# Kernel tuning notes

Measured on AMD Instinct MI355X. Metric: run time of the kernel, lower is better.

## Reference

```python
import jax, jax.numpy as jnp
import numpy as np

B, N, D, E, H, K = 2, 2048, 1024, 8, 2048, 2


def setup_inputs() -> dict:
    key = jax.random.key(0)
    ks = jax.random.split(key, 5)
    s = 0.02  # init scale
    return {
        "x": jax.random.normal(ks[0], (B, N, D), dtype=jnp.float32),
        "w_gate": jax.random.normal(ks[1], (D, E), dtype=jnp.float32) * s,
        "b_gate": jnp.zeros((E,), dtype=jnp.float32),
        "w1": jax.random.normal(ks[2], (E, D, H), dtype=jnp.float32) * s,
        "b1": jnp.zeros((E, H), dtype=jnp.float32),
        "w2": jax.random.normal(ks[3], (E, H, D), dtype=jnp.float32) * s,
        "b2": jnp.zeros((E, D), dtype=jnp.float32),
    }


def reference(x, w_gate, b_gate, w1, b1, w2, b2):
    b, n, d = x.shape
    T = b * n
    xf = x.reshape(T, d)                                   # (T, D)
    # --- top-k routing ---
    logits = xf @ w_gate + b_gate                          # (T, E)
    topk_logits, topk_idx = jax.lax.top_k(logits, K)       # (T, K)
    topk_gates = jax.nn.softmax(topk_logits, axis=-1)      # softmax over selected experts
    entropy = -(topk_gates * jnp.log(jnp.clip(topk_gates, 1e-8, None))).sum(-1).mean()
    # scatter top-k gates into full (T, E) gate matrix (zeros for unselected)
    gates = jnp.zeros_like(logits).at[jnp.arange(T)[:, None], topk_idx].add(topk_gates)
    # --- expert MLPs (dense over experts; gates zero out unselected) ---
    h = jax.nn.relu(jnp.einsum('td,edh->eth', xf, w1) + b1[:, None, :])  # (E, T, H)
    y = jnp.einsum('eth,ehd->etd', h, w2) + b2[:, None, :]               # (E, T, D)
    out = jnp.einsum('etd,te->td', y, gates).reshape(b, n, d)
    return out, entropy
```

## Files before the change

kernel.cpp:

```cpp
#include <hip/hip_runtime.h>

#define T_TOK 4096
#define D_DIM 1024
#define E_EXP 8
#define H_DIM 2048
#define CAP   9216
#define TILES_M 72

typedef __attribute__((ext_vector_type(8))) short bf16x8;
typedef __attribute__((ext_vector_type(4))) float f32x4;

__device__ inline unsigned short f2bf(float f) {
    unsigned int u = __float_as_uint(f);
    unsigned int r = (u + 0x7fffu + ((u >> 16) & 1u)) >> 16;
    return (unsigned short)r;
}

#define GLD_LDS16(g, l)                                                        \
    __builtin_amdgcn_global_load_lds(                                          \
        (const __attribute__((address_space(1))) void*)(g),                    \
        (__attribute__((address_space(3))) void*)(l), 16, 0, 0)

__global__ __launch_bounds__(256) void tcvt_kernel(const float* __restrict__ src,
                                                   unsigned short* __restrict__ dst,
                                                   int R, int C) {
    __shared__ float tile[64][65];
    size_t eo = (size_t)blockIdx.z * R * C;
    src += eo; dst += eo;
    int tx = threadIdx.x & 15, ty = threadIdx.x >> 4;
    int c0 = blockIdx.x * 64, r0 = blockIdx.y * 64;
    #pragma unroll
    for (int i = 0; i < 4; i++) {
        int row = ty + i * 16;
        float4 v = *(const float4*)&src[(size_t)(r0 + row) * C + c0 + tx * 4];
        tile[row][tx * 4 + 0] = v.x;
        tile[row][tx * 4 + 1] = v.y;
        tile[row][tx * 4 + 2] = v.z;
        tile[row][tx * 4 + 3] = v.w;
    }
    __syncthreads();
    #pragma unroll
    for (int i = 0; i < 4; i++) {
        int cc = ty + i * 16;
        int rr = tx * 4;
        ushort4 o;
        o.x = f2bf(tile[rr + 0][cc]);
        o.y = f2bf(tile[rr + 1][cc]);
        o.z = f2bf(tile[rr + 2][cc]);
        o.w = f2bf(tile[rr + 3][cc]);
        *(ushort4*)&dst[(size_t)(c0 + cc) * R + r0 + rr] = o;
    }
}

__global__ __launch_bounds__(256) void gating_kernel(
    const float* __restrict__ xf, const float* __restrict__ wg,
    const float* __restrict__ bg, unsigned short* __restrict__ xb,
    int* __restrict__ tk_e, float* __restrict__ tk_g,
    float* __restrict__ ent_part)
{
    __shared__ float ents[4];
    int wave = threadIdx.x >> 6, lane = threadIdx.x & 63;
    int t = blockIdx.x * 4 + wave;
    const float* xr = xf + (size_t)t * D_DIM;
    unsigned short* xbr = xb + (size_t)t * D_DIM;
    float acc[8] = {0.f,0.f,0.f,0.f,0.f,0.f,0.f,0.f};
    for (int i = 0; i < 16; i++) {
        int d = lane + i * 64;
        float xv = xr[d];
        xbr[d] = f2bf(xv);
        const float4* wr = (const float4*)(wg + (size_t)d * 8);
        float4 w0 = wr[0], w1 = wr[1];
        acc[0] += xv * w0.x; acc[1] += xv * w0.y; acc[2] += xv * w0.z; acc[3] += xv * w0.w;
        acc[4] += xv * w1.x; acc[5] += xv * w1.y; acc[6] += xv * w1.z; acc[7] += xv * w1.w;
    }
    #pragma unroll
    for (int s = 1; s < 64; s <<= 1) {
        #pragma unroll
        for (int e = 0; e < 8; e++) acc[e] += __shfl_xor(acc[e], s, 64);
    }
    if (lane == 0) {
        float l[8];
        #pragma unroll
        for (int e = 0; e < 8; e++) l[e] = acc[e] + bg[e];
        int i0 = 0;
        #pragma unroll
        for (int e = 1; e < 8; e++) if (l[e] > l[i0]) i0 = e;
        int i1 = (i0 == 0) ? 1 : 0;
        #pragma unroll
        for (int e = 0; e < 8; e++) if (e != i0 && l[e] > l[i1]) i1 = e;
        float z  = expf(l[i1] - l[i0]);
        float p0 = 1.0f / (1.0f + z);
        float p1 = z / (1.0f + z);
        float ent = -(p0 * logf(fmaxf(p0, 1e-8f)) + p1 * logf(fmaxf(p1, 1e-8f)));
        ents[wave] = ent;
        tk_e[t * 2 + 0] = i0; tk_g[t * 2 + 0] = p0;
        tk_e[t * 2 + 1] = i1; tk_g[t * 2 + 1] = p1;
    }
    __syncthreads();
    if (threadIdx.x == 0)
        ent_part[blockIdx.x] = ents[0] + ents[1] + ents[2] + ents[3];
}

__global__ __launch_bounds__(1024) void route_kernel(
    const int* __restrict__ tk_e, const float* __restrict__ tk_g,
    int* __restrict__ off, int* __restrict__ slot_token,
    float* __restrict__ slot_gate, int* __restrict__ slot_of,
    const float* __restrict__ ent_part, float* __restrict__ ent_out)
{
    __shared__ int wt[16][8];
    __shared__ int wx[16][8];
    __shared__ int base[9];
    __shared__ int tot[8];
    __shared__ float es[16];

    int tid = threadIdx.x, wid = tid >> 6, lane = tid & 63;
    int i0 = tid * 8;
    int ev[8];
    *(int4*)&ev[0] = *(const int4*)&tk_e[i0];
    *(int4*)&ev[4] = *(const int4*)&tk_e[i0 + 4];

    float s = ent_part[tid];
    #pragma unroll
    for (int d = 1; d < 64; d <<= 1) s += __shfl_xor(s, d, 64);
    if (lane == 0) es[wid] = s;

    unsigned own[4] = {0u, 0u, 0u, 0u};
    #pragma unroll
    for (int j = 0; j < 8; j++) {
        int e = ev[j];
        int reg = ((e < 4) ? 0 : 2) + (e & 1);
        own[reg] += 1u << (((e >> 1) & 1) * 16);
    }
    unsigned inc[4] = {own[0], own[1], own[2], own[3]};
    #pragma unroll
    for (int d = 1; d < 64; d <<= 1) {
        #pragma unroll
        for (int k = 0; k < 4; k++) {
            unsigned t = __shfl_up(inc[k], d, 64);
            if (lane >= d) inc[k] += t;
        }
    }
    if (lane == 63) {
        #pragma unroll
        for (int e = 0; e < 8; e++) {
            int reg = ((e < 4) ? 0 : 2) + (e & 1);
            wt[wid][e] = (inc[reg] >> (((e >> 1) & 1) * 16)) & 0xFFFF;
        }
    }
    __syncthreads();
    if (tid == 0) {
        int o = 0;
        for (int e = 0; e < 8; e++) {
            int run = 0;
            for (int w = 0; w < 16; w++) { wx[w][e] = run; run += wt[w][e]; }
            tot[e] = run;
            base[e] = o;
            off[e] = o;
            o += (run + 127) & ~127;
        }
        base[8] = o;
        off[8] = o;
        float se = 0.f;
        for (int w = 0; w < 16; w++) se += es[w];
        *ent_out = se * (1.0f / T_TOK);
    }
    __syncthreads();

    #pragma unroll
    for (int e = 0; e < 8; e++) {
        int p0 = base[e] + tot[e], p1 = base[e + 1];
        for (int i = p0 + tid; i < p1; i += 1024) slot_token[i] = -1;
    }

    unsigned run[4] = {0u, 0u, 0u, 0u};
    #pragma unroll
    for (int j = 0; j < 8; j++) {
        int e = ev[j];
        int reg = ((e < 4) ? 0 : 2) + (e & 1);
        int sh = ((e >> 1) & 1) * 16;
        int lx = (int)(((inc[reg] - own[reg]) >> sh) & 0xFFFF);
        int lr = (int)((run[reg] >> sh) & 0xFFFF);
        int slot = base[e] + wx[wid][e] + lx + lr;
        run[reg] += 1u << sh;
        int i = i0 + j;
        slot_token[slot] = i >> 1;
        slot_gate[slot] = tk_g[i];
        slot_of[i] = slot;
    }
}

template<int KD, int ND, bool GATHER, bool RELU>
__global__ __launch_bounds__(256) void gemm2p_kernel(
    const unsigned short* __restrict__ Ag, const unsigned short* __restrict__ Bw,
    const float* __restrict__ bias, const int* __restrict__ off,
    const int* __restrict__ slot_token, unsigned short* __restrict__ Out)
{
    __shared__ __align__(16) unsigned short As[2][128 * 32];
    __shared__ __align__(16) unsigned short Bs[2][128 * 32];

    int nwgx = gridDim.x;
    int nwg = nwgx * gridDim.y;
    int orig = blockIdx.y * nwgx + blockIdx.x;
    int q = nwg >> 3, r = nwg & 7;
    int xcd = orig & 7, idx = orig >> 3;
    int nid = (xcd < r ? xcd * (q + 1) : r * (q + 1) + (xcd - r) * q) + idx;
    int bx = nid % nwgx, by = nid / nwgx;

    int s0 = bx * 128;
    if (s0 >= off[E_EXP]) return;
    int e = 0;
    while (s0 >= off[e + 1]) e++;
    int n0 = by * 128;

    int tid = threadIdx.x;
    int wave = tid >> 6, lane = tid & 63;
    int lrow = lane & 15, quad = lane >> 4;
    int srow = lane >> 2;
    int scol = ((lane & 3) ^ ((srow >> 1) & 3)) * 8;

    int r0 = 16 * wave + srow, r1 = r0 + 64;
    const unsigned short* a0;
    const unsigned short* a1;
    if constexpr (GATHER) {
        int t0 = slot_token[s0 + r0]; if (t0 < 0) t0 = 0;
        int t1 = slot_token[s0 + r1]; if (t1 < 0) t1 = 0;
        a0 = Ag + (size_t)t0 * KD + scol;
        a1 = Ag + (size_t)t1 * KD + scol;
    } else {
        a0 = Ag + (size_t)(s0 + r0) * KD + scol;
        a1 = Ag + (size_t)(s0 + r1) * KD + scol;
    }
    const unsigned short* wb = Bw + (size_t)e * ND * KD;
    const unsigned short* bp0 = wb + (size_t)(n0 + r0) * KD + scol;
    const unsigned short* bp1 = wb + (size_t)(n0 + r1) * KD + scol;

    int stA0 = (16 * wave) * 32;
    int stA1 = (64 + 16 * wave) * 32;

    f32x4 acc[4][4];
    #pragma unroll
    for (int mi = 0; mi < 4; mi++)
        #pragma unroll
        for (int ni = 0; ni < 4; ni++) acc[mi][ni] = (f32x4){0.f, 0.f, 0.f, 0.f};

    int wr = (wave >> 1) * 64, wc = (wave & 1) * 64;
    int g = (quad ^ ((lrow >> 1) & 3)) * 8;

    GLD_LDS16(a0,  &As[0][stA0]);
    GLD_LDS16(a1,  &As[0][stA1]);
    GLD_LDS16(bp0, &Bs[0][stA0]);
    GLD_LDS16(bp1, &Bs[0][stA1]);
    __syncthreads();

    constexpr int NT = KD / 32;
    int cur = 0;
    for (int t = 0; t < NT - 1; ++t) {
        int nb = cur ^ 1;
        int k1 = (t + 1) * 32;
        GLD_LDS16(a0 + k1,  &As[nb][stA0]);
        GLD_LDS16(a1 + k1,  &As[nb][stA1]);
        GLD_LDS16(bp0 + k1, &Bs[nb][stA0]);
        GLD_LDS16(bp1 + k1, &Bs[nb][stA1]);
        bf16x8 af[4], bfr[4];
        #pragma unroll
        for (int i = 0; i < 4; i++) {
            af[i]  = *(const bf16x8*)&As[cur][(wr + i * 16 + lrow) * 32 + g];
            bfr[i] = *(const bf16x8*)&Bs[cur][(wc + i * 16 + lrow) * 32 + g];
        }
        #pragma unroll
        for (int mi = 0; mi < 4; mi++)
            #pragma unroll
            for (int ni = 0; ni < 4; ni++)
                acc[mi][ni] = __builtin_amdgcn_mfma_f32_16x16x32_bf16(
                    af[mi], bfr[ni], acc[mi][ni], 0, 0, 0);
        __syncthreads();
        cur = nb;
    }
    {
        bf16x8 af[4], bfr[4];
        #pragma unroll
        for (int i = 0; i < 4; i++) {
            af[i]  = *(const bf16x8*)&As[cur][(wr + i * 16 + lrow) * 32 + g];
            bfr[i] = *(const bf16x8*)&Bs[cur][(wc + i * 16 + lrow) * 32 + g];
        }
        #pragma unroll
        for (int mi = 0; mi < 4; mi++)
            #pragma unroll
            for (int ni = 0; ni < 4; ni++)
                acc[mi][ni] = __builtin_amdgcn_mfma_f32_16x16x32_bf16(
                    af[mi], bfr[ni], acc[mi][ni], 0, 0, 0);
    }

    float bv[4];
    #pragma unroll
    for (int ni = 0; ni < 4; ni++)
        bv[ni] = bias[(size_t)e * ND + n0 + wc + ni * 16 + lrow];
    unsigned short* w = &As[0][0] + wave * 1024;
    __syncthreads();
    #pragma unroll
    for (int mi = 0; mi < 4; mi++) {
        #pragma unroll
        for (int ni = 0; ni < 4; ni++)
            #pragma unroll
            for (int rr = 0; rr < 4; rr++) {
                float v = acc[mi][ni][rr] + bv[ni];
                if constexpr (RELU) v = fmaxf(v, 0.0f);
                w[(quad * 4 + rr) * 64 + ni * 16 + lrow] = f2bf(v);
            }
        int rd = lane >> 3, cc = (lane & 7) * 8;
        bf16x8 v0 = *(const bf16x8*)&w[rd * 64 + cc];
        bf16x8 v1 = *(const bf16x8*)&w[(8 + rd) * 64 + cc];
        size_t rowg = (size_t)(s0 + wr + mi * 16 + rd) * ND + n0 + wc + cc;
        *(bf16x8*)&Out[rowg] = v0;
        *(bf16x8*)&Out[rowg + 8 * (size_t)ND] = v1;
    }
}

__global__ __launch_bounds__(256) void combine_kernel(
    const unsigned short* __restrict__ Yb, const int* __restrict__ slot_of,
    const float* __restrict__ tk_g, float* __restrict__ out)
{
    int t = blockIdx.x * 2 + (threadIdx.x >> 7);
    int j = threadIdx.x & 127;
    int sA = slot_of[t * 2], sB = slot_of[t * 2 + 1];
    float gA = tk_g[t * 2], gB = tk_g[t * 2 + 1];
    uint4 va = *(const uint4*)(Yb + (size_t)sA * D_DIM + j * 8);
    uint4 vb = *(const uint4*)(Yb + (size_t)sB * D_DIM + j * 8);
    const unsigned int* pa = (const unsigned int*)&va;
    const unsigned int* pb = (const unsigned int*)&vb;
    float o[8];
    #pragma unroll
    for (int i = 0; i < 4; i++) {
        float a_lo = __uint_as_float(pa[i] << 16);
        float a_hi = __uint_as_float(pa[i] & 0xffff0000u);
        float b_lo = __uint_as_float(pb[i] << 16);
        float b_hi = __uint_as_float(pb[i] & 0xffff0000u);
        o[i * 2 + 0] = gA * a_lo + gB * b_lo;
        o[i * 2 + 1] = gA * a_hi + gB * b_hi;
    }
    float* op = out + (size_t)t * D_DIM + j * 8;
    ((float4*)op)[0] = make_float4(o[0], o[1], o[2], o[3]);
    ((float4*)op)[1] = make_float4(o[4], o[5], o[6], o[7]);
}

extern "C" void kernel_launch(void* const* d_in, const int* in_sizes, int n_in,
                              void* d_out, int out_size, void* d_ws, size_t ws_size,
                              hipStream_t stream)
{
    const float* xf = (const float*)d_in[0];
    const float* wg = (const float*)d_in[1];
    const float* bg = (const float*)d_in[2];
    const float* w1 = (const float*)d_in[3];
    const float* b1 = (const float*)d_in[4];
    const float* w2 = (const float*)d_in[5];
    const float* b2 = (const float*)d_in[6];
    float* out = (float*)d_out;

    char* p = (char*)d_ws;
    int* off    = (int*)p;
    int* tk_e   = off + 16;
    float* tk_g = (float*)(tk_e + T_TOK * 2);
    int* slot_token = (int*)(tk_g + T_TOK * 2);
    float* slot_gate = (float*)(slot_token + CAP);
    int* slot_of = (int*)(slot_gate + CAP);
    float* ent_part = (float*)(slot_of + T_TOK * 2);
    size_t ofs = ((size_t)((char*)(ent_part + T_TOK / 4) - p) + 255) & ~(size_t)255;
    unsigned short* xb  = (unsigned short*)(p + ofs); ofs += (size_t)T_TOK * D_DIM * 2;
    unsigned short* w1t = (unsigned short*)(p + ofs); ofs += (size_t)E_EXP * D_DIM * H_DIM * 2;
    unsigned short* w2t = (unsigned short*)(p + ofs); ofs += (size_t)E_EXP * H_DIM * D_DIM * 2;
    unsigned short* Hb  = (unsigned short*)(p + ofs); ofs += (size_t)CAP * H_DIM * 2;
    unsigned short* Yb  = w1t;

    gating_kernel<<<T_TOK / 4, 256, 0, stream>>>(xf, wg, bg, xb, tk_e, tk_g, ent_part);
    route_kernel<<<1, 1024, 0, stream>>>(tk_e, tk_g, off, slot_token, slot_gate, slot_of,
                                         ent_part, out + (size_t)T_TOK * D_DIM);
    tcvt_kernel<<<dim3(H_DIM / 64, D_DIM / 64, E_EXP), 256, 0, stream>>>(w1, w1t, D_DIM, H_DIM);
    tcvt_kernel<<<dim3(D_DIM / 64, H_DIM / 64, E_EXP), 256, 0, stream>>>(w2, w2t, H_DIM, D_DIM);
    gemm2p_kernel<D_DIM, H_DIM, true, true>
        <<<dim3(TILES_M, H_DIM / 128), 256, 0, stream>>>(xb, w1t, b1, off, slot_token, Hb);
    gemm2p_kernel<H_DIM, D_DIM, false, false>
        <<<dim3(TILES_M, D_DIM / 128), 256, 0, stream>>>(Hb, w2t, b2, off, slot_token, Yb);
    combine_kernel<<<T_TOK / 2, 256, 0, stream>>>(Yb, slot_of, tk_g, out);
}
```

Measured before the change: 371.1 us.

## Deepen grouped GEMM K-tile to 64 with two-ahead prefetch and fine waitcnt sync

The expert GEMM kernel now stages 64-wide K tiles with an 8-chunk XOR swizzle and issues two stages before starting compute. Each iteration waits with a partial vmcnt so the next tile's loads stay in flight, and raw s_barrier replaces __syncthreads. It also raises MFMA priority around the math block, requests two blocks per CU in launch bounds, and drops the XCD-aware block remapping. The aim is to hide global-to-LDS latency and halve barrier count, at the cost of doubled LDS (64KB per block) and possibly worse L2 locality without the remap.

```diff
diff --git a/kernel.cpp b/kernel.cpp
--- a/kernel.cpp
+++ b/kernel.cpp
@@ -190,52 +190,41 @@
 }
 
 template<int KD, int ND, bool GATHER, bool RELU>
-__global__ __launch_bounds__(256) void gemm2p_kernel(
+__global__ __launch_bounds__(256, 2) void gemmk_kernel(
     const unsigned short* __restrict__ Ag, const unsigned short* __restrict__ Bw,
     const float* __restrict__ bias, const int* __restrict__ off,
     const int* __restrict__ slot_token, unsigned short* __restrict__ Out)
 {
-    __shared__ __align__(16) unsigned short As[2][128 * 32];
-    __shared__ __align__(16) unsigned short Bs[2][128 * 32];
-
-    int nwgx = gridDim.x;
-    int nwg = nwgx * gridDim.y;
-    int orig = blockIdx.y * nwgx + blockIdx.x;
-    int q = nwg >> 3, r = nwg & 7;
-    int xcd = orig & 7, idx = orig >> 3;
-    int nid = (xcd < r ? xcd * (q + 1) : r * (q + 1) + (xcd - r) * q) + idx;
-    int bx = nid % nwgx, by = nid / nwgx;
-
-    int s0 = bx * 128;
+    constexpr int NT = KD / 64;
+    __shared__ __align__(16) unsigned short As[2][128 * 64];
+    __shared__ __align__(16) unsigned short Bs[2][128 * 64];
+
+    int s0 = blockIdx.x * 128;
     if (s0 >= off[E_EXP]) return;
     int e = 0;
     while (s0 >= off[e + 1]) e++;
-    int n0 = by * 128;
+    int n0 = blockIdx.y * 128;
 
     int tid = threadIdx.x;
-    int wave = tid >> 6, lane = tid & 63;
+    int w = tid >> 6, lane = tid & 63;
+    int wm = w >> 1, wn = w & 1;
     int lrow = lane & 15, quad = lane >> 4;
-    int srow = lane >> 2;
-    int scol = ((lane & 3) ^ ((srow >> 1) & 3)) * 8;
-
-    int r0 = 16 * wave + srow, r1 = r0 + 64;
-    const unsigned short* a0;
-    const unsigned short* a1;
-    if constexpr (GATHER) {
-        int t0 = slot_token[s0 + r0]; if (t0 < 0) t0 = 0;
-        int t1 = slot_token[s0 + r1]; if (t1 < 0) t1 = 0;
-        a0 = Ag + (size_t)t0 * KD + scol;
-        a1 = Ag + (size_t)t1 * KD + scol;
-    } else {
-        a0 = Ag + (size_t)(s0 + r0) * KD + scol;
-        a1 = Ag + (size_t)(s0 + r1) * KD + scol;
-    }
-    const unsigned short* wb = Bw + (size_t)e * ND * KD;
-    const unsigned short* bp0 = wb + (size_t)(n0 + r0) * KD + scol;
-    const unsigned short* bp1 = wb + (size_t)(n0 + r1) * KD + scol;
-
-    int stA0 = (16 * wave) * 32;
-    int stA1 = (64 + 16 * wave) * 32;
+
+    int gchunk = ((lane & 7) ^ (lane >> 3)) * 8;
+    const unsigned short* ap[4];
+    const unsigned short* bp[4];
+    const unsigned short* wbp = Bw + (size_t)e * ND * KD;
+    #pragma unroll
+    for (int i = 0; i < 4; i++) {
+        int row = i * 32 + w * 8 + (lane >> 3);
+        if constexpr (GATHER) {
+            int t0 = slot_token[s0 + row]; if (t0 < 0) t0 = 0;
+            ap[i] = Ag + (size_t)t0 * KD + gchunk;
+        } else {
+            ap[i] = Ag + (size_t)(s0 + row) * KD + gchunk;
+        }
+        bp[i] = wbp + (size_t)(n0 + row) * KD + gchunk;
+    }
 
     f32x4 acc[4][4];
     #pragma unroll
@@ -243,60 +232,63 @@
         #pragma unroll
         for (int ni = 0; ni < 4; ni++) acc[mi][ni] = (f32x4){0.f, 0.f, 0.f, 0.f};
 
-    int wr = (wave >> 1) * 64, wc = (wave & 1) * 64;
-    int g = (quad ^ ((lrow >> 1) & 3)) * 8;
-
-    GLD_LDS16(a0,  &As[0][stA0]);
-    GLD_LDS16(a1,  &As[0][stA1]);
-    GLD_LDS16(bp0, &Bs[0][stA0]);
-    GLD_LDS16(bp1, &Bs[0][stA1]);
-    __syncthreads();
-
-    constexpr int NT = KD / 32;
-    int cur = 0;
+    auto STAGE = [&](int b, int ku) {
+        int koff = ku * 64;
+        #pragma unroll
+        for (int i = 0; i < 4; i++) {
+            GLD_LDS16(ap[i] + koff, &As[b][i * 2048 + w * 512]);
+            GLD_LDS16(bp[i] + koff, &Bs[b][i * 2048 + w * 512]);
+        }
+    };
+
+    auto COMPUTE = [&](int b) {
+        bf16x8 af[4][2], bfr[4][2];
+        #pragma unroll
+        for (int mi = 0; mi < 4; mi++) {
+            int row = wm * 64 + mi * 16 + lrow;
+            int rb = row * 64, sw = row & 7;
+            af[mi][0] = *(const bf16x8*)&As[b][rb + ((quad    ) ^ sw) * 8];
+            af[mi][1] = *(const bf16x8*)&As[b][rb + ((quad + 4) ^ sw) * 8];
+        }
+        #pragma unroll
+        for (int ni = 0; ni < 4; ni++) {
+            int row = wn * 64 + ni * 16 + lrow;
+            int rb = row * 64, sw = row & 7;
+            bfr[ni][0] = *(const bf16x8*)&Bs[b][rb + ((quad    ) ^ sw) * 8];
+            bfr[ni][1] = *(const bf16x8*)&Bs[b][rb + ((quad + 4) ^ sw) * 8];
+        }
+        __builtin_amdgcn_s_setprio(1);
+        #pragma unroll
+        for (int ks = 0; ks < 2; ks++)
+            #pragma unroll
+            for (int mi = 0; mi < 4; mi++)
+                #pragma unroll
+                for (int ni = 0; ni < 4; ni++)
+                    acc[mi][ni] = __builtin_amdgcn_mfma_f32_16x16x32_bf16(
+                        af[mi][ks], bfr[ni][ks], acc[mi][ni], 0, 0, 0);
+        __builtin_amdgcn_s_setprio(0);
+    };
+
+    STAGE(0, 0);
+    STAGE(1, 1);
     for (int t = 0; t < NT - 1; ++t) {
-        int nb = cur ^ 1;
-        int k1 = (t + 1) * 32;
-        GLD_LDS16(a0 + k1,  &As[nb][stA0]);
-        GLD_LDS16(a1 + k1,  &As[nb][stA1]);
-        GLD_LDS16(bp0 + k1, &Bs[nb][stA0]);
-        GLD_LDS16(bp1 + k1, &Bs[nb][stA1]);
-        bf16x8 af[4], bfr[4];
-        #pragma unroll
-        for (int i = 0; i < 4; i++) {
-            af[i]  = *(const bf16x8*)&As[cur][(wr + i * 16 + lrow) * 32 + g];
-            bfr[i] = *(const bf16x8*)&Bs[cur][(wc + i * 16 + lrow) * 32 + g];
-        }
-        #pragma unroll
-        for (int mi = 0; mi < 4; mi++)
-            #pragma unroll
-            for (int ni = 0; ni < 4; ni++)
-                acc[mi][ni] = __builtin_amdgcn_mfma_f32_16x16x32_bf16(
-                    af[mi], bfr[ni], acc[mi][ni], 0, 0, 0);
-        __syncthreads();
-        cur = nb;
-    }
-    {
-        bf16x8 af[4], bfr[4];
-        #pragma unroll
-        for (int i = 0; i < 4; i++) {
-            af[i]  = *(const bf16x8*)&As[cur][(wr + i * 16 + lrow) * 32 + g];
-            bfr[i] = *(const bf16x8*)&Bs[cur][(wc + i * 16 + lrow) * 32 + g];
-        }
-        #pragma unroll
-        for (int mi = 0; mi < 4; mi++)
-            #pragma unroll
-            for (int ni = 0; ni < 4; ni++)
-                acc[mi][ni] = __builtin_amdgcn_mfma_f32_16x16x32_bf16(
-                    af[mi], bfr[ni], acc[mi][ni], 0, 0, 0);
-    }
-
+        asm volatile("s_waitcnt vmcnt(8)" ::: "memory");
+        asm volatile("s_barrier" ::: "memory");
+        COMPUTE(t & 1);
+        asm volatile("s_barrier" ::: "memory");
+        if (t + 2 < NT) STAGE(t & 1, t + 2);
+    }
+    asm volatile("s_waitcnt vmcnt(0)" ::: "memory");
+    asm volatile("s_barrier" ::: "memory");
+    COMPUTE((NT - 1) & 1);
+    asm volatile("s_barrier" ::: "memory");
+
+    int wr = wm * 64, wc = wn * 64;
     float bv[4];
     #pragma unroll
     for (int ni = 0; ni < 4; ni++)
         bv[ni] = bias[(size_t)e * ND + n0 + wc + ni * 16 + lrow];
-    unsigned short* w = &As[0][0] + wave * 1024;
-    __syncthreads();
+    unsigned short* scr = &As[0][0] + w * 1024;
     #pragma unroll
     for (int mi = 0; mi < 4; mi++) {
         #pragma unroll
@@ -305,11 +297,11 @@
             for (int rr = 0; rr < 4; rr++) {
                 float v = acc[mi][ni][rr] + bv[ni];
                 if constexpr (RELU) v = fmaxf(v, 0.0f);
-                w[(quad * 4 + rr) * 64 + ni * 16 + lrow] = f2bf(v);
+                scr[(quad * 4 + rr) * 64 + ni * 16 + lrow] = f2bf(v);
             }
         int rd = lane >> 3, cc = (lane & 7) * 8;
-        bf16x8 v0 = *(const bf16x8*)&w[rd * 64 + cc];
-        bf16x8 v1 = *(const bf16x8*)&w[(8 + rd) * 64 + cc];
+        bf16x8 v0 = *(const bf16x8*)&scr[rd * 64 + cc];
+        bf16x8 v1 = *(const bf16x8*)&scr[(8 + rd) * 64 + cc];
         size_t rowg = (size_t)(s0 + wr + mi * 16 + rd) * ND + n0 + wc + cc;
         *(bf16x8*)&Out[rowg] = v0;
         *(bf16x8*)&Out[rowg + 8 * (size_t)ND] = v1;
@@ -376,9 +368,9 @@
                                          ent_part, out + (size_t)T_TOK * D_DIM);
     tcvt_kernel<<<dim3(H_DIM / 64, D_DIM / 64, E_EXP), 256, 0, stream>>>(w1, w1t, D_DIM, H_DIM);
     tcvt_kernel<<<dim3(D_DIM / 64, H_DIM / 64, E_EXP), 256, 0, stream>>>(w2, w2t, H_DIM, D_DIM);
-    gemm2p_kernel<D_DIM, H_DIM, true, true>
+    gemmk_kernel<D_DIM, H_DIM, true, true>
         <<<dim3(TILES_M, H_DIM / 128), 256, 0, stream>>>(xb, w1t, b1, off, slot_token, Hb);
-    gemm2p_kernel<H_DIM, D_DIM, false, false>
+    gemmk_kernel<H_DIM, D_DIM, false, false>
         <<<dim3(TILES_M, D_DIM / 128), 256, 0, stream>>>(Hb, w2t, b2, off, slot_token, Yb);
     combine_kernel<<<T_TOK / 2, 256, 0, stream>>>(Yb, slot_of, tk_g, out);
 }
```

Result: faster. 336.7 us (-9.3%).

## Prefetch two K-tiles ahead with manual waitcnt/barriers and drop XCD remap

Applied to the files above, without the earlier changes.

Restructures the GEMM main loop so two K-tiles are issued up front, and each iteration waits with vmcnt(4) instead of a full drain, so one tile's loads stay in flight during compute. It also raises wave priority around the MFMA block with s_setprio. The XCD-aware block index remapping is removed in favour of plain blockIdx order, which changes L2 locality across chiplets. The hand-written waitcnt/barrier sequence relies on the compiler not reordering LDS reads, which adds correctness risk.

```diff
diff --git a/kernel.cpp b/kernel.cpp
--- a/kernel.cpp
+++ b/kernel.cpp
@@ -190,27 +190,20 @@
 }
 
 template<int KD, int ND, bool GATHER, bool RELU>
-__global__ __launch_bounds__(256) void gemm2p_kernel(
+__global__ __launch_bounds__(256) void gemm_kernel(
     const unsigned short* __restrict__ Ag, const unsigned short* __restrict__ Bw,
     const float* __restrict__ bias, const int* __restrict__ off,
     const int* __restrict__ slot_token, unsigned short* __restrict__ Out)
 {
+    constexpr int NT = KD / 32;
     __shared__ __align__(16) unsigned short As[2][128 * 32];
     __shared__ __align__(16) unsigned short Bs[2][128 * 32];
 
-    int nwgx = gridDim.x;
-    int nwg = nwgx * gridDim.y;
-    int orig = blockIdx.y * nwgx + blockIdx.x;
-    int q = nwg >> 3, r = nwg & 7;
-    int xcd = orig & 7, idx = orig >> 3;
-    int nid = (xcd < r ? xcd * (q + 1) : r * (q + 1) + (xcd - r) * q) + idx;
-    int bx = nid % nwgx, by = nid / nwgx;
-
-    int s0 = bx * 128;
+    int s0 = blockIdx.x * 128;
     if (s0 >= off[E_EXP]) return;
     int e = 0;
     while (s0 >= off[e + 1]) e++;
-    int n0 = by * 128;
+    int n0 = blockIdx.y * 128;
 
     int tid = threadIdx.x;
     int wave = tid >> 6, lane = tid & 63;
@@ -246,57 +239,48 @@
     int wr = (wave >> 1) * 64, wc = (wave & 1) * 64;
     int g = (quad ^ ((lrow >> 1) & 3)) * 8;
 
-    GLD_LDS16(a0,  &As[0][stA0]);
-    GLD_LDS16(a1,  &As[0][stA1]);
-    GLD_LDS16(bp0, &Bs[0][stA0]);
-    GLD_LDS16(bp1, &Bs[0][stA1]);
-    __syncthreads();
-
-    constexpr int NT = KD / 32;
-    int cur = 0;
-    for (int t = 0; t < NT - 1; ++t) {
-        int nb = cur ^ 1;
-        int k1 = (t + 1) * 32;
-        GLD_LDS16(a0 + k1,  &As[nb][stA0]);
-        GLD_LDS16(a1 + k1,  &As[nb][stA1]);
-        GLD_LDS16(bp0 + k1, &Bs[nb][stA0]);
-        GLD_LDS16(bp1 + k1, &Bs[nb][stA1]);
+    auto STAGE = [&](int b, int k) {
+        GLD_LDS16(a0 + k,  &As[b][stA0]);
+        GLD_LDS16(a1 + k,  &As[b][stA1]);
+        GLD_LDS16(bp0 + k, &Bs[b][stA0]);
+        GLD_LDS16(bp1 + k, &Bs[b][stA1]);
+    };
+    auto COMPUTE = [&](int b) {
         bf16x8 af[4], bfr[4];
         #pragma unroll
         for (int i = 0; i < 4; i++) {
-            af[i]  = *(const bf16x8*)&As[cur][(wr + i * 16 + lrow) * 32 + g];
-            bfr[i] = *(const bf16x8*)&Bs[cur][(wc + i * 16 + lrow) * 32 + g];
+            af[i]  = *(const bf16x8*)&As[b][(wr + i * 16 + lrow) * 32 + g];
+            bfr[i] = *(const bf16x8*)&Bs[b][(wc + i * 16 + lrow) * 32 + g];
         }
+        __builtin_amdgcn_s_setprio(1);
         #pragma unroll
         for (int mi = 0; mi < 4; mi++)
             #pragma unroll
             for (int ni = 0; ni < 4; ni++)
                 acc[mi][ni] = __builtin_amdgcn_mfma_f32_16x16x32_bf16(
                     af[mi], bfr[ni], acc[mi][ni], 0, 0, 0);
-        __syncthreads();
-        cur = nb;
-    }
-    {
-        bf16x8 af[4], bfr[4];
-        #pragma unroll
-        for (int i = 0; i < 4; i++) {
-            af[i]  = *(const bf16x8*)&As[cur][(wr + i * 16 + lrow) * 32 + g];
-            bfr[i] = *(const bf16x8*)&Bs[cur][(wc + i * 16 + lrow) * 32 + g];
-        }
-        #pragma unroll
-        for (int mi = 0; mi < 4; mi++)
-            #pragma unroll
-            for (int ni = 0; ni < 4; ni++)
-                acc[mi][ni] = __builtin_amdgcn_mfma_f32_16x16x32_bf16(
-                    af[mi], bfr[ni], acc[mi][ni], 0, 0, 0);
-    }
+        __builtin_amdgcn_s_setprio(0);
+    };
+
+    STAGE(0, 0);
+    STAGE(1, 32);
+    for (int t = 0; t < NT - 1; ++t) {
+        asm volatile("s_waitcnt vmcnt(4)" ::: "memory");
+        asm volatile("s_barrier" ::: "memory");
+        COMPUTE(t & 1);
+        asm volatile("s_barrier" ::: "memory");
+        if (t + 2 < NT) STAGE(t & 1, (t + 2) * 32);
+    }
+    asm volatile("s_waitcnt vmcnt(0)" ::: "memory");
+    asm volatile("s_barrier" ::: "memory");
+    COMPUTE((NT - 1) & 1);
+    asm volatile("s_barrier" ::: "memory");
 
     float bv[4];
     #pragma unroll
     for (int ni = 0; ni < 4; ni++)
         bv[ni] = bias[(size_t)e * ND + n0 + wc + ni * 16 + lrow];
     unsigned short* w = &As[0][0] + wave * 1024;
-    __syncthreads();
     #pragma unroll
     for (int mi = 0; mi < 4; mi++) {
         #pragma unroll
@@ -376,9 +360,9 @@
                                          ent_part, out + (size_t)T_TOK * D_DIM);
     tcvt_kernel<<<dim3(H_DIM / 64, D_DIM / 64, E_EXP), 256, 0, stream>>>(w1, w1t, D_DIM, H_DIM);
     tcvt_kernel<<<dim3(D_DIM / 64, H_DIM / 64, E_EXP), 256, 0, stream>>>(w2, w2t, H_DIM, D_DIM);
-    gemm2p_kernel<D_DIM, H_DIM, true, true>
+    gemm_kernel<D_DIM, H_DIM, true, true>
         <<<dim3(TILES_M, H_DIM / 128), 256, 0, stream>>>(xb, w1t, b1, off, slot_token, Hb);
-    gemm2p_kernel<H_DIM, D_DIM, false, false>
+    gemm_kernel<H_DIM, D_DIM, false, false>
         <<<dim3(TILES_M, D_DIM / 128), 256, 0, stream>>>(Hb, w2t, b2, off, slot_token, Yb);
     combine_kernel<<<T_TOK / 2, 256, 0, stream>>>(Yb, slot_of, tk_g, out);
 }
```

Measured after the change: 331.4 us. 10.7% less time.
